# Kernel optimization log

Measured on AMD Instinct MI355X. Metric: run time of the kernel, lower is better.

Reference implementation:

```python
import jax, jax.numpy as jnp
import numpy as np

PI = 3.1415  # matches the literal constant in the source


def setup_inputs() -> dict:
    key = jax.random.key(0)
    nt, ns, nh = 1024, 2048, 32
    k1, k2, k3, k4, k5 = jax.random.split(key, 5)
    P = jax.random.uniform(k1, (nt, ns), dtype=jnp.float32) * 10.0           # precipitation >= 0
    T1 = jax.random.normal(k2, (nt, ns), dtype=jnp.float32) * 10.0           # daily min temp
    T2 = T1 + jax.random.uniform(k3, (nt, ns), dtype=jnp.float32) * 15.0 + 0.5  # max temp > min temp
    E = jax.random.uniform(k4, (nt, ns), dtype=jnp.float32) * 5.0            # potential ET >= 0
    w = jax.random.uniform(k5, (nh * 4,), dtype=jnp.float32, minval=-1.0, maxval=1.0)
    return {"P": P, "T1": T1, "T2": T2, "E": E, "w": w}


def reference(P, T1, T2, E, w):
    nt, ns = P.shape
    nh = w.shape[0] // 4

    # rain/snow partition. arccos argument is clipped for numerical safety; the
    # clipped region (|ratio|>1) is exactly where rP is overwritten by the masks,
    # so forward values match the original exactly.
    Ta = (T1 + T2) * 0.5
    ratio = jnp.clip((T1 + T2) / (T2 - T1), -1.0, 1.0)
    rP = 1.0 - jnp.arccos(ratio) / PI
    rP = jnp.where(T1 >= 0, 1.0, rP)
    rP = jnp.where(T2 <= 0, 0.0, rP)
    Ps = (1.0 - rP) * P   # snow
    Pl = rP * P           # liquid rain

    gm = jnp.exp(w[:nh]) + 1.0            # melt factor, [nh]
    ge = jax.nn.sigmoid(w[nh:2 * nh])     # ET gate, [nh]
    go = jax.nn.sigmoid(w[2 * nh:3 * nh]) # outflow gate, [nh]
    ga = jax.nn.softmax(w[3 * nh:])       # mixing weights (Dropout in eval mode = identity), [nh]

    def step(carry, xs):
        S0, H0 = carry                    # each [ns, nh]
        Ta_k, Ps_k, Pl_k, E_k = xs        # each [ns]
        Sm = jnp.minimum(S0, jnp.maximum(Ta_k[:, None] * gm, 0.0))  # snowmelt
        S = S0 + Ps_k[:, None]
        H = jnp.maximum(H0 + Sm + Pl_k[:, None] - E_k[:, None] * ge, 0.0)
        Q = H * go
        Y = jnp.sum(Q * ga, axis=1)       # [ns]
        return (S - Sm, H - Q), Y

    init = (jnp.zeros((ns, nh), P.dtype), jnp.zeros((ns, nh), P.dtype))
    _, Yout = jax.lax.scan(step, init, (Ta, Ps, Pl, E))
    return Yout  # [nt, ns]
```

## Files before the change

### kernel.cpp

```cpp
#include <hip/hip_runtime.h>

#define NT 1024
#define NS 2048
#define NH 32
#define PF 8

__global__ __launch_bounds__(256, 1)
void waternet_kernel(const float* __restrict__ P,
                     const float* __restrict__ T1,
                     const float* __restrict__ T2,
                     const float* __restrict__ E,
                     const float* __restrict__ w,
                     float* __restrict__ Y)
{
    const int tid  = threadIdx.x;
    const int lane = tid & 31;
    const int grp  = tid >> 5;

    const int bid    = blockIdx.x;
    const int sChunk = (bid & 7) * 32 + (bid >> 3);
    const int s      = sChunk * 8 + grp;

    const float wm = w[lane];
    const float we = w[NH + lane];
    const float wo = w[2 * NH + lane];
    const float wa = w[3 * NH + lane];

    const float gm = expf(wm) + 1.0f;
    const float ge = 1.0f / (1.0f + expf(-we));
    const float go = 1.0f / (1.0f + expf(-wo));

    float mx = wa;
    #pragma unroll
    for (int o = 16; o; o >>= 1) mx = fmaxf(mx, __shfl_xor(mx, o));
    float ea = expf(wa - mx);
    float ssum = ea;
    #pragma unroll
    for (int o = 16; o; o >>= 1) ssum += __shfl_xor(ssum, o);
    const float ga  = ea / ssum;
    const float go1 = 1.0f - go;
    const float gq  = go * ga;

    float S  = 0.0f;
    float Hs = 0.0f;

    __shared__ float4 stage[2][8][32];
    __shared__ float  ytmp[8][32][33];

    size_t base = (size_t)lane * NS + s;
    float p0 = P[base], a0 = T1[base], b0 = T2[base], e0 = E[base];
    size_t bn = base + (size_t)32 * NS;
    float pg = P[bn], ag = T1[bn], bg = T2[bn], eg = E[bn];

    auto prep = [&](float p, float ta, float tb, float ee, int buf) {
        float sum   = ta + tb;
        float ratio = sum / (tb - ta);
        ratio = fminf(fmaxf(ratio, -1.0f), 1.0f);
        float rP = 1.0f - acosf(ratio) * (1.0f / 3.1415f);
        if (ta >= 0.0f) rP = 1.0f;
        if (tb <= 0.0f) rP = 0.0f;
        float Pl  = rP * p;
        float Ps  = p - Pl;
        float TaP = fmaxf(sum * 0.5f, 0.0f);
        stage[buf][grp][lane] = make_float4(TaP, Ps, Pl, ee);
    };

    prep(p0, a0, b0, e0, 0);

    float xx[PF], xy[PF], xw[PF];
    #pragma unroll
    for (int j = 0; j < PF; ++j) {
        float4 x = stage[0][grp][j];
        xx[j] = x.x * gm;
        xy[j] = x.y;
        xw[j] = x.z - x.w * ge;
    }

    #pragma unroll 2
    for (int c = 0; c < 32; ++c) {
        if (c < 31) prep(pg, ag, bg, eg, (c + 1) & 1);
        if (c < 30) {
            size_t nb = base + (size_t)(c + 2) * 32 * NS;
            pg = P[nb]; ag = T1[nb]; bg = T2[nb]; eg = E[nb];
        }

        #pragma unroll
        for (int k = 0; k < 32; ++k) {
            const int sl = k & (PF - 1);
            const float bm = xx[sl], Ps = xy[sl], pw = xw[sl];
            const float Sm = fminf(S, bm);
            const float t  = Hs + pw;
            const float Sn = (S + Ps) - Sm;
            const float h3 = fmaxf(t + Sm, 0.0f);
            S  = Sn;
            Hs = h3 * go1;
            ytmp[grp][k][lane] = h3 * gq;

            const int idx = k + PF;
            const int buf = (c + (idx >> 5)) & 1;
            float4 x = stage[buf][grp][idx & 31];
            xx[sl] = x.x * gm;
            xy[sl] = x.y;
            xw[sl] = x.z - x.w * ge;
        }

        float r0 = 0.f, r1 = 0.f, r2 = 0.f, r3 = 0.f;
        #pragma unroll
        for (int k = 0; k < 32; k += 4) {
            r0 += ytmp[grp][lane][k + 0];
            r1 += ytmp[grp][lane][k + 1];
            r2 += ytmp[grp][lane][k + 2];
            r3 += ytmp[grp][lane][k + 3];
        }
        Y[(size_t)(c * 32 + lane) * NS + s] = (r0 + r1) + (r2 + r3);
    }
}

extern "C" void kernel_launch(void* const* d_in, const int* in_sizes, int n_in,
                              void* d_out, int out_size, void* d_ws, size_t ws_size,
                              hipStream_t stream) {
    const float* P  = (const float*)d_in[0];
    const float* T1 = (const float*)d_in[1];
    const float* T2 = (const float*)d_in[2];
    const float* E  = (const float*)d_in[3];
    const float* w  = (const float*)d_in[4];
    float* Y = (float*)d_out;

    waternet_kernel<<<dim3(256), dim3(256), 0, stream>>>(P, T1, T2, E, w, Y);
}
```

Before: 47.75 us.

## Bulk-load stage chunk into registers and double-buffer output reduction

```diff
diff --git a/kernel.cpp b/kernel.cpp
--- a/kernel.cpp
+++ b/kernel.cpp
@@ -3,7 +3,6 @@
 #define NT 1024
 #define NS 2048
 #define NH 32
-#define PF 8
 
 __global__ __launch_bounds__(256, 1)
 void waternet_kernel(const float* __restrict__ P,
@@ -45,7 +44,7 @@
     float Hs = 0.0f;
 
     __shared__ float4 stage[2][8][32];
-    __shared__ float  ytmp[8][32][33];
+    __shared__ float  ytmp[2][8][32][33];
 
     size_t base = (size_t)lane * NS + s;
     float p0 = P[base], a0 = T1[base], b0 = T2[base], e0 = E[base];
@@ -67,52 +66,58 @@
 
     prep(p0, a0, b0, e0, 0);
 
-    float xx[PF], xy[PF], xw[PF];
-    #pragma unroll
-    for (int j = 0; j < PF; ++j) {
-        float4 x = stage[0][grp][j];
-        xx[j] = x.x * gm;
-        xy[j] = x.y;
-        xw[j] = x.z - x.w * ge;
-    }
+    for (int c = 0; c < 32; ++c) {
+        float4 x[32];
+        #pragma unroll
+        for (int j = 0; j < 32; ++j) x[j] = stage[c & 1][grp][j];
 
-    #pragma unroll 2
-    for (int c = 0; c < 32; ++c) {
         if (c < 31) prep(pg, ag, bg, eg, (c + 1) & 1);
         if (c < 30) {
             size_t nb = base + (size_t)(c + 2) * 32 * NS;
             pg = P[nb]; ag = T1[nb]; bg = T2[nb]; eg = E[nb];
         }
 
+        if (c > 0) {
+            const float* yr = &ytmp[(c - 1) & 1][grp][lane][0];
+            float r0 = 0.f, r1 = 0.f, r2 = 0.f, r3 = 0.f;
+            #pragma unroll
+            for (int k = 0; k < 32; k += 4) {
+                r0 += yr[k + 0];
+                r1 += yr[k + 1];
+                r2 += yr[k + 2];
+                r3 += yr[k + 3];
+            }
+            Y[(size_t)((c - 1) * 32 + lane) * NS + s] = (r0 + r1) + (r2 + r3);
+        }
+
+        float* yw = &ytmp[c & 1][grp][0][lane];
         #pragma unroll
         for (int k = 0; k < 32; ++k) {
-            const int sl = k & (PF - 1);
-            const float bm = xx[sl], Ps = xy[sl], pw = xw[sl];
+            const float4 xx = x[k];
+            const float bm = xx.x * gm;
+            const float pw = fmaf(-xx.w, ge, xx.z);
             const float Sm = fminf(S, bm);
-            const float t  = Hs + pw;
-            const float Sn = (S + Ps) - Sm;
-            const float h3 = fmaxf(t + Sm, 0.0f);
-            S  = Sn;
+            const float Sp = S + xx.y;
+            const float h3 = fmaxf(Hs + (pw + Sm), 0.0f);
+            S  = Sp - Sm;
             Hs = h3 * go1;
-            ytmp[grp][k][lane] = h3 * gq;
-
-            const int idx = k + PF;
-            const int buf = (c + (idx >> 5)) & 1;
-            float4 x = stage[buf][grp][idx & 31];
-            xx[sl] = x.x * gm;
-            xy[sl] = x.y;
-            xw[sl] = x.z - x.w * ge;
+            yw[k * 33] = h3 * gq;
         }
 
+        asm volatile("" ::: "memory");
+    }
+
+    {
+        const float* yr = &ytmp[1][grp][lane][0];
         float r0 = 0.f, r1 = 0.f, r2 = 0.f, r3 = 0.f;
         #pragma unroll
         for (int k = 0; k < 32; k += 4) {
-            r0 += ytmp[grp][lane][k + 0];
-            r1 += ytmp[grp][lane][k + 1];
-            r2 += ytmp[grp][lane][k + 2];
-            r3 += ytmp[grp][lane][k + 3];
+            r0 += yr[k + 0];
+            r1 += yr[k + 1];
+            r2 += yr[k + 2];
+            r3 += yr[k + 3];
         }
-        Y[(size_t)(c * 32 + lane) * NS + s] = (r0 + r1) + (r2 + r3);
+        Y[(size_t)(31 * 32 + lane) * NS + s] = (r0 + r1) + (r2 + r3);
     }
 }
 
```

New measurement: 45.74 us. 4.2% less time.
